# Performance work log

Hardware: AMD Instinct MI355X
Metric: run time of the kernel (lower is better)

Reference implementation:

```python
import jax, jax.numpy as jnp
import numpy as np

B, S, D, H = 2, 2048, 4096, 32
HD = D // H  # 128

def _rope(t, cos, sin):
    # t: [B,S,H,HD]; cos,sin: [S,HD//2]; interleaved complex pairs on last dim
    b, s, h, d = t.shape
    tr = t.reshape(b, s, h, d // 2, 2)
    x0, x1 = tr[..., 0], tr[..., 1]
    c = cos[None, :, None, :]
    sn = sin[None, :, None, :]
    o0 = x0 * c - x1 * sn
    o1 = x0 * sn + x1 * c
    return jnp.stack([o0, o1], axis=-1).reshape(b, s, h, d)

def setup_inputs() -> dict:
    key = jax.random.key(0)
    ks = jax.random.split(key, 6)
    x = jax.random.normal(ks[0], (B, S, D), dtype=jnp.float32)
    theta = 10000.0 ** (-jnp.arange(0, HD, 2, dtype=jnp.float32) / HD)  # [HD//2]
    ang = jnp.arange(S, dtype=jnp.float32)[:, None] * theta[None, :]    # [S, HD//2]
    freqs_cos, freqs_sin = jnp.cos(ang), jnp.sin(ang)
    # additive causal mask [S,S]
    mask = jnp.where(jnp.triu(jnp.ones((S, S), dtype=bool), k=1), -1e9, 0.0).astype(jnp.float32)
    std = 1.0 / np.sqrt(D)
    wq = jax.random.normal(ks[1], (D, D), dtype=jnp.float32) * std
    wk = jax.random.normal(ks[2], (D, D), dtype=jnp.float32) * std
    wv = jax.random.normal(ks[3], (D, D), dtype=jnp.float32) * std
    wo = jax.random.normal(ks[4], (D, D), dtype=jnp.float32) * std
    return {"x": x, "freqs_cos": freqs_cos, "freqs_sin": freqs_sin, "mask": mask,
            "wq": wq, "wk": wk, "wv": wv, "wo": wo, "start_pos": 0}

def reference(x, freqs_cos, freqs_sin, mask, wq, wk, wv, wo, start_pos):
    b, s, d = x.shape
    # Linear layers: torch nn.Linear stores weight [out,in] -> x @ W.T
    xq = (x @ wq.T).reshape(b, s, H, HD)
    xk = (x @ wk.T).reshape(b, s, H, HD)
    xv = (x @ wv.T).reshape(b, s, H, HD)
    xq = _rope(xq, freqs_cos, freqs_sin)
    xk = _rope(xk, freqs_cos, freqs_sin)
    # prefill (start_pos=0): cache slice [:, :s] == xk, xv
    scale = 1.0 / jnp.sqrt(jnp.float32(HD))
    scores = jnp.einsum("bqhd,bkhd->bhqk", xq, xk) * scale + mask[None, None, :, :]
    probs = jax.nn.softmax(scores, axis=-1)
    out = jnp.einsum("bhqk,bkhd->bqhd", probs, xv).reshape(b, s, d)
    return out @ wo.T
```

## Files before the change

### kernel.cpp

```cpp
#include <hip/hip_runtime.h>
#include <hip/hip_bf16.h>
#include <math.h>

typedef unsigned short u16;
typedef __bf16 bf16x8 __attribute__((ext_vector_type(8)));
typedef float f32x4 __attribute__((ext_vector_type(4)));

#define B_  2
#define S_  2048
#define D_  4096
#define H_  32
#define HD_ 128

__device__ __forceinline__ unsigned rne_bf16(float x) {
  unsigned u = __float_as_uint(x);
  return (u + 0x7fffu + ((u >> 16) & 1u)) >> 16;
}

__device__ __forceinline__ void async16(void* lds_p, const void* g) {
  __builtin_amdgcn_global_load_lds(
      (__attribute__((address_space(1))) void*)(g),
      (__attribute__((address_space(3))) void*)(lds_p), 16, 0, 0);
}

__global__ __launch_bounds__(256) void convert_bf16(
    const float* __restrict__ src, u16* __restrict__ dst, int n8) {
  int i = blockIdx.x * 256 + threadIdx.x;
  if (i >= n8) return;
  const float4* s = (const float4*)src + (size_t)i * 2;
  float4 a = s[0], b = s[1];
  uint4 o;
  o.x = rne_bf16(a.x) | (rne_bf16(a.y) << 16);
  o.y = rne_bf16(a.z) | (rne_bf16(a.w) << 16);
  o.z = rne_bf16(b.x) | (rne_bf16(b.y) << 16);
  o.w = rne_bf16(b.z) | (rne_bf16(b.w) << 16);
  ((uint4*)dst)[i] = o;
}

template <int MODE>
__global__ __launch_bounds__(256, 3) void gemm_bt(
    const u16* __restrict__ A, const u16* __restrict__ Bw,
    u16* __restrict__ outB, float* __restrict__ outF,
    const float* __restrict__ fc, const float* __restrict__ fs) {
  __shared__ __align__(16) u16 lds[16384];
  const int tid  = threadIdx.x;
  const int lane = tid & 63;
  const int wave = tid >> 6;
  const int lm   = lane & 15, quad = lane >> 4;
  const int mr = (wave >> 1) * 64, nc = (wave & 1) * 64;
  const int K = 4096;
  const int NT = K / 32;

  const int bid = blockIdx.y * 32 + blockIdx.x;
  const int xg = bid & 7, l = bid >> 3;
  const int m0 = (((xg & 3) * 8) + (l & 7)) * 128;
  const int n0 = (((xg >> 2) * 16) + (l >> 3)) * 128;

  const int ca = tid, cb = tid + 256;
  const int ra = ca >> 2, ga = ((ca & 3) ^ ((ca >> 3) & 3)) * 8;
  const int rb = cb >> 2, gb = ((cb & 3) ^ ((cb >> 3) & 3)) * 8;
  const u16* Ag0 = A + (size_t)(m0 + ra) * K + ga;
  const u16* Ag1 = A + (size_t)(m0 + rb) * K + gb;
  const u16* Bg0 = Bw + (size_t)(n0 + ra) * K + ga;
  const u16* Bg1 = Bw + (size_t)(n0 + rb) * K + gb;

  const int koff = (quad ^ ((lm >> 1) & 3)) * 8;

  f32x4 acc[4][4] = {};

  async16(&lds[ca * 8], Ag0);
  async16(&lds[cb * 8], Ag1);
  async16(&lds[4096 + ca * 8], Bg0);
  async16(&lds[4096 + cb * 8], Bg1);
  __syncthreads();

  for (int t = 0; t < NT; ++t) {
    const u16* As = lds + (t & 1) * 8192;
    const u16* Bs = As + 4096;
    if (t < NT - 1) {
      u16* Ld = lds + ((t + 1) & 1) * 8192;
      const size_t ko = (size_t)(t + 1) * 32;
      async16(&Ld[ca * 8], Ag0 + ko);
      async16(&Ld[cb * 8], Ag1 + ko);
      async16(&Ld[4096 + ca * 8], Bg0 + ko);
      async16(&Ld[4096 + cb * 8], Bg1 + ko);
    }
    bf16x8 af[4], bfr[4];
#pragma unroll
    for (int i = 0; i < 4; ++i) af[i] = *(const bf16x8*)&As[(mr + i * 16 + lm) * 32 + koff];
#pragma unroll
    for (int j = 0; j < 4; ++j) bfr[j] = *(const bf16x8*)&Bs[(nc + j * 16 + lm) * 32 + koff];
#pragma unroll
    for (int i = 0; i < 4; ++i)
#pragma unroll
      for (int j = 0; j < 4; ++j)
        acc[i][j] = __builtin_amdgcn_mfma_f32_16x16x32_bf16(af[i], bfr[j], acc[i][j], 0, 0, 0);
    __syncthreads();
  }

  if (MODE == 1) {
#pragma unroll
    for (int i = 0; i < 4; ++i) {
      const int mbase = m0 + mr + i * 16 + quad * 4;
#pragma unroll
      for (int j = 0; j < 4; ++j) {
        const int n = n0 + nc + j * 16 + lm;
        const int h = n >> 7, d = n & 127, ir = d >> 1;
#pragma unroll
        for (int r = 0; r < 4; ++r) {
          const int m = mbase + r;
          const int s = m & (S_ - 1);
          const int bb = m >> 11;
          float v = acc[i][j][r];
          float p = __shfl_xor(v, 1);
          float cv = fc[s * (HD_ / 2) + ir];
          float sv = fs[s * (HD_ / 2) + ir];
          float o = ((lane & 1) == 0) ? (v * cv - p * sv) : (p * sv + v * cv);
          float po = __shfl_xor(o, 1);
          if ((lane & 1) == 0) {
            unsigned pkt = rne_bf16(o) | (rne_bf16(po) << 16);
            size_t idx = (((size_t)(bb * H_ + h) * S_ + s) * HD_ + d) >> 1;
            ((unsigned*)outB)[idx] = pkt;
          }
        }
      }
    }
  } else if (MODE == 3) {
#pragma unroll
    for (int i = 0; i < 4; ++i) {
      const int mbase = m0 + mr + i * 16 + quad * 4;
      const int s0 = mbase & (S_ - 1);
      const int bb = mbase >> 11;
#pragma unroll
      for (int j = 0; j < 4; ++j) {
        const int n = n0 + nc + j * 16 + lm;
        const int h = n >> 7, d = n & 127;
        uint2 pkt;
        pkt.x = rne_bf16(acc[i][j][0]) | (rne_bf16(acc[i][j][1]) << 16);
        pkt.y = rne_bf16(acc[i][j][2]) | (rne_bf16(acc[i][j][3]) << 16);
        size_t idx = ((size_t)(bb * H_ + h) * HD_ + d) * S_ + s0;
        *(uint2*)&outB[idx] = pkt;
      }
    }
  } else {
#pragma unroll
    for (int i = 0; i < 4; ++i) {
      const int mbase = m0 + mr + i * 16 + quad * 4;
#pragma unroll
      for (int j = 0; j < 4; ++j) {
        const int n = n0 + nc + j * 16 + lm;
#pragma unroll
        for (int r = 0; r < 4; ++r) outF[(size_t)(mbase + r) * D_ + n] = acc[i][j][r];
      }
    }
  }
}

__global__ __launch_bounds__(256, 2) void flash_attn(
    const u16* __restrict__ Qb, const u16* __restrict__ Kb,
    const u16* __restrict__ Vtb, u16* __restrict__ attn) {
  __shared__ __align__(16) u16 lds[32768];

  const int tid = threadIdx.x;
  const int lane = tid & 63, w = tid >> 6;
  const int lm = lane & 15, quad = lane >> 4;
  const int qb = 15 - blockIdx.x;
  const int bh = blockIdx.y;
  const int bb = bh >> 5, h = bh & 31;

  const u16* Qg = Qb + ((size_t)bh * S_ + qb * 128 + w * 32) * HD_;
  const u16* Kg = Kb + (size_t)bh * S_ * HD_;
  const u16* Vg = Vtb + (size_t)bh * HD_ * S_;

  const u16* kp[4];
  const u16* vp[4];
#pragma unroll
  for (int it = 0; it < 4; ++it) {
    int c = tid + 256 * it;
    int kr = c >> 4, kc = (c & 15) ^ (kr & 15);
    kp[it] = Kg + (size_t)kr * HD_ + kc * 8;
    int vr = c >> 3, vc = (c & 7) ^ (vr & 7);
    vp[it] = Vg + (size_t)vr * S_ + vc * 8;
  }

  bf16x8 qf[2][4];
#pragma unroll
  for (int qt = 0; qt < 2; ++qt)
#pragma unroll
    for (int dk = 0; dk < 4; ++dk)
      qf[qt][dk] = *(const bf16x8*)(Qg + (size_t)(qt * 16 + lm) * HD_ + dk * 32 + quad * 8);

  f32x4 accO[8][2] = {};
  float m_run[2] = {-1e30f, -1e30f}, l_run[2] = {0.f, 0.f};
  const float scale = 0.08838834764831845f;
  const int nkt = 2 * qb + 2;
  const int qg0 = qb * 128 + w * 32;
  const int wq_max = qg0 + 31;

#pragma unroll
  for (int it = 0; it < 4; ++it) {
    async16(&lds[(tid + 256 * it) * 8], kp[it]);
    async16(&lds[8192 + (tid + 256 * it) * 8], vp[it]);
  }

  for (int kt = 0; kt < nkt; ++kt) {
    const int k0 = kt * 64;
    const int cur = (kt & 1) * 16384;
    __syncthreads();
    if (kt + 1 < nkt) {
      const int nxt = cur ^ 16384;
      const size_t koK = (size_t)(kt + 1) * 64 * HD_;
      const size_t koV = (size_t)(kt + 1) * 64;
#pragma unroll
      for (int it = 0; it < 4; ++it) {
        async16(&lds[nxt + (tid + 256 * it) * 8], kp[it] + koK);
        async16(&lds[nxt + 8192 + (tid + 256 * it) * 8], vp[it] + koV);
      }
    }
    if (k0 <= wq_max) {
      const u16* Ks = lds + cur;
      const u16* Vts = lds + cur + 8192;
      f32x4 sacc[2][4] = {};
#pragma unroll
      for (int dk = 0; dk < 4; ++dk) {
        bf16x8 kf[4];
#pragma unroll
        for (int t = 0; t < 4; ++t) {
          int row = (t >> 1) * 32 + ((lm >> 2) * 8) + ((t & 1) * 4) + (lm & 3);
          int ch = (dk * 4 + quad) ^ (row & 15);
          kf[t] = *(const bf16x8*)&Ks[(row * 16 + ch) * 8];
        }
#pragma unroll
        for (int t = 0; t < 4; ++t)
#pragma unroll
          for (int qt = 0; qt < 2; ++qt)
            sacc[qt][t] = __builtin_amdgcn_mfma_f32_16x16x32_bf16(kf[t], qf[qt][dk], sacc[qt][t], 0, 0, 0);
      }
      if (k0 + 63 > qg0) {
#pragma unroll
        for (int qt = 0; qt < 2; ++qt) {
          int q = qg0 + qt * 16 + lm;
#pragma unroll
          for (int t = 0; t < 4; ++t) {
            int kb = k0 + (t >> 1) * 32 + quad * 8 + (t & 1) * 4;
#pragma unroll
            for (int r = 0; r < 4; ++r)
              if (kb + r > q) sacc[qt][t][r] = -1e30f;
          }
        }
      }
      bf16x8 pf[2][2];
      float alpha[2];
#pragma unroll
      for (int qt = 0; qt < 2; ++qt) {
        float tmax = sacc[qt][0][0];
#pragma unroll
        for (int t = 0; t < 4; ++t)
#pragma unroll
          for (int r = 0; r < 4; ++r) tmax = fmaxf(tmax, sacc[qt][t][r]);
        tmax = fmaxf(tmax, __shfl_xor(tmax, 16));
        tmax = fmaxf(tmax, __shfl_xor(tmax, 32));
        float mnew = fmaxf(m_run[qt], tmax);
        alpha[qt] = __expf((m_run[qt] - mnew) * scale);
        m_run[qt] = mnew;
        float ms = mnew * scale;
        float rs = 0.f;
#pragma unroll
        for (int t = 0; t < 4; ++t)
#pragma unroll
          for (int r = 0; r < 4; ++r) {
            float p = __expf(fmaf(sacc[qt][t][r], scale, -ms));
            sacc[qt][t][r] = p;
            rs += p;
          }
        rs += __shfl_xor(rs, 16);
        rs += __shfl_xor(rs, 32);
        l_run[qt] = l_run[qt] * alpha[qt] + rs;
#pragma unroll
        for (int kc = 0; kc < 2; ++kc)
#pragma unroll
          for (int j = 0; j < 4; ++j) {
            pf[kc][qt][j]     = (__bf16)sacc[qt][2 * kc][j];
            pf[kc][qt][j + 4] = (__bf16)sacc[qt][2 * kc + 1][j];
          }
      }
#pragma unroll
      for (int dt = 0; dt < 8; ++dt)
#pragma unroll
        for (int qt = 0; qt < 2; ++qt)
#pragma unroll
          for (int r = 0; r < 4; ++r) accO[dt][qt][r] *= alpha[qt];
#pragma unroll
      for (int kc = 0; kc < 2; ++kc)
#pragma unroll
        for (int dt = 0; dt < 8; ++dt) {
          int row = dt * 16 + lm;
          int ch = (kc * 4 + quad) ^ (row & 7);
          bf16x8 vf = *(const bf16x8*)&Vts[(row * 8 + ch) * 8];
#pragma unroll
          for (int qt = 0; qt < 2; ++qt)
            accO[dt][qt] = __builtin_amdgcn_mfma_f32_16x16x32_bf16(vf, pf[kc][qt], accO[dt][qt], 0, 0, 0);
        }
    }
  }

  __syncthreads();
  u16* Et = lds;
  float inv[2] = {1.f / l_run[0], 1.f / l_run[1]};
#pragma unroll
  for (int dt = 0; dt < 8; ++dt)
#pragma unroll
    for (int qt = 0; qt < 2; ++qt) {
      const int rowq = w * 32 + qt * 16 + lm;
#pragma unroll
      for (int rp = 0; rp < 2; ++rp) {
        float a0 = accO[dt][qt][rp * 2] * inv[qt];
        float a1 = accO[dt][qt][rp * 2 + 1] * inv[qt];
        unsigned pkt = rne_bf16(a0) | (rne_bf16(a1) << 16);
        *(unsigned*)&Et[rowq * 136 + dt * 16 + quad * 4 + rp * 2] = pkt;
      }
    }
  const int rloc = w * 32 + (lane >> 1);
  const int half = lane & 1;
  const size_t gbase = (size_t)(bb * S_ + qb * 128 + rloc) * D_ + h * 128 + half * 64;
#pragma unroll
  for (int k = 0; k < 8; ++k) {
    uint4 vv = *(const uint4*)&Et[rloc * 136 + half * 64 + k * 8];
    *(uint4*)&attn[gbase + k * 8] = vv;
  }
}

extern "C" void kernel_launch(void* const* d_in, const int* in_sizes, int n_in,
                              void* d_out, int out_size, void* d_ws, size_t ws_size,
                              hipStream_t stream) {
  const float* x  = (const float*)d_in[0];
  const float* fc = (const float*)d_in[1];
  const float* fs = (const float*)d_in[2];
  const float* wq = (const float*)d_in[4];
  const float* wk = (const float*)d_in[5];
  const float* wv = (const float*)d_in[6];
  const float* wo = (const float*)d_in[7];
  float* out = (float*)d_out;

  char* ws = (char*)d_ws;
  const size_t SZ = (size_t)B_ * S_ * D_ * 2;
  u16* xb  = (u16*)(ws);
  u16* wqb = (u16*)(ws + SZ);
  u16* wkb = (u16*)(ws + 2 * SZ);
  u16* wvb = (u16*)(ws + 3 * SZ);
  u16* Qb  = (u16*)(ws + 4 * SZ);
  u16* Kb  = (u16*)(ws + 5 * SZ);
  u16* Vtb = (u16*)(ws + 6 * SZ);
  u16* attn = xb;
  u16* wob  = wqb;

  dim3 blk(256);
  const int n8 = (B_ * S_ * D_) / 8;
  convert_bf16<<<n8 / 256, blk, 0, stream>>>(x, xb, n8);
  convert_bf16<<<n8 / 256, blk, 0, stream>>>(wq, wqb, n8);
  convert_bf16<<<n8 / 256, blk, 0, stream>>>(wk, wkb, n8);
  convert_bf16<<<n8 / 256, blk, 0, stream>>>(wv, wvb, n8);

  dim3 g1(32, 32);
  gemm_bt<1><<<g1, blk, 0, stream>>>(xb, wqb, Qb, nullptr, fc, fs);
  gemm_bt<1><<<g1, blk, 0, stream>>>(xb, wkb, Kb, nullptr, fc, fs);
  gemm_bt<3><<<g1, blk, 0, stream>>>(xb, wvb, Vtb, nullptr, nullptr, nullptr);

  dim3 g2(16, 64);
  flash_attn<<<g2, blk, 0, stream>>>(Qb, Kb, Vtb, attn);

  convert_bf16<<<n8 / 256, blk, 0, stream>>>(wo, wob, n8);
  gemm_bt<4><<<g1, blk, 0, stream>>>(attn, wob, nullptr, out, nullptr, nullptr);
}
```

Before: 1.126 ms.

## Triple-buffer GEMM loads, lazy softmax rescale, MFMA priority, batch conversions

The GEMM moves from double to triple-buffered LDS staging, prefetching two K-tiles ahead and waiting with explicit vmcnt counts and raw barriers instead of __syncthreads. Flash attention now rescales the running max and accumulators only when any lane's new tile max exceeds the old one by a threshold, and raises wave priority around the MFMA blocks. The four input fp32-to-bf16 conversions are merged into one launch. Together these aim to hide load latency, skip per-tile rescale work and cut launch overhead. The costs are higher LDS use per GEMM block, which may lower occupancy, and the risk that a stale running max lets exp values grow within the threshold bound.

```diff
diff --git a/kernel.cpp b/kernel.cpp
--- a/kernel.cpp
+++ b/kernel.cpp
@@ -37,12 +37,32 @@
   ((uint4*)dst)[i] = o;
 }
 
+__global__ __launch_bounds__(256) void convert_bf16_x4(
+    const float* __restrict__ s0, const float* __restrict__ s1,
+    const float* __restrict__ s2, const float* __restrict__ s3,
+    u16* __restrict__ d0, u16* __restrict__ d1,
+    u16* __restrict__ d2, u16* __restrict__ d3) {
+  const int per = (B_ * S_ * D_) / 8 / 256;
+  const int which = blockIdx.x / per;
+  const int i = (blockIdx.x % per) * 256 + threadIdx.x;
+  const float* src = which == 0 ? s0 : which == 1 ? s1 : which == 2 ? s2 : s3;
+  u16* dst = which == 0 ? d0 : which == 1 ? d1 : which == 2 ? d2 : d3;
+  const float4* s = (const float4*)src + (size_t)i * 2;
+  float4 a = s[0], b = s[1];
+  uint4 o;
+  o.x = rne_bf16(a.x) | (rne_bf16(a.y) << 16);
+  o.y = rne_bf16(a.z) | (rne_bf16(a.w) << 16);
+  o.z = rne_bf16(b.x) | (rne_bf16(b.y) << 16);
+  o.w = rne_bf16(b.z) | (rne_bf16(b.w) << 16);
+  ((uint4*)dst)[i] = o;
+}
+
 template <int MODE>
 __global__ __launch_bounds__(256, 3) void gemm_bt(
     const u16* __restrict__ A, const u16* __restrict__ Bw,
     u16* __restrict__ outB, float* __restrict__ outF,
     const float* __restrict__ fc, const float* __restrict__ fs) {
-  __shared__ __align__(16) u16 lds[16384];
+  __shared__ __align__(16) u16 lds[24576];
   const int tid  = threadIdx.x;
   const int lane = tid & 63;
   const int wave = tid >> 6;
@@ -68,23 +88,25 @@
 
   f32x4 acc[4][4] = {};
 
-  async16(&lds[ca * 8], Ag0);
-  async16(&lds[cb * 8], Ag1);
-  async16(&lds[4096 + ca * 8], Bg0);
-  async16(&lds[4096 + cb * 8], Bg1);
-  __syncthreads();
-
+#define GSTAGE(BUF, T) do {                                   \
+    u16* Ld_ = lds + (BUF) * 8192;                            \
+    const size_t ko_ = (size_t)(T) * 32;                      \
+    async16(&Ld_[ca * 8], Ag0 + ko_);                         \
+    async16(&Ld_[cb * 8], Ag1 + ko_);                         \
+    async16(&Ld_[4096 + ca * 8], Bg0 + ko_);                  \
+    async16(&Ld_[4096 + cb * 8], Bg1 + ko_);                  \
+  } while (0)
+
+  GSTAGE(0, 0);
+  GSTAGE(1, 1);
+  asm volatile("s_waitcnt vmcnt(4)" ::: "memory");
+  asm volatile("s_barrier" ::: "memory");
+
+  int rbuf = 0, sbuf = 2;
   for (int t = 0; t < NT; ++t) {
-    const u16* As = lds + (t & 1) * 8192;
+    const u16* As = lds + rbuf * 8192;
     const u16* Bs = As + 4096;
-    if (t < NT - 1) {
-      u16* Ld = lds + ((t + 1) & 1) * 8192;
-      const size_t ko = (size_t)(t + 1) * 32;
-      async16(&Ld[ca * 8], Ag0 + ko);
-      async16(&Ld[cb * 8], Ag1 + ko);
-      async16(&Ld[4096 + ca * 8], Bg0 + ko);
-      async16(&Ld[4096 + cb * 8], Bg1 + ko);
-    }
+    if (t + 2 < NT) GSTAGE(sbuf, t + 2);
     bf16x8 af[4], bfr[4];
 #pragma unroll
     for (int i = 0; i < 4; ++i) af[i] = *(const bf16x8*)&As[(mr + i * 16 + lm) * 32 + koff];
@@ -95,8 +117,18 @@
 #pragma unroll
       for (int j = 0; j < 4; ++j)
         acc[i][j] = __builtin_amdgcn_mfma_f32_16x16x32_bf16(af[i], bfr[j], acc[i][j], 0, 0, 0);
-    __syncthreads();
-  }
+    if (t < NT - 1) {
+      if (t + 2 < NT) {
+        asm volatile("s_waitcnt vmcnt(4)" ::: "memory");
+      } else {
+        asm volatile("s_waitcnt vmcnt(0)" ::: "memory");
+      }
+      asm volatile("s_barrier" ::: "memory");
+    }
+    rbuf = rbuf == 2 ? 0 : rbuf + 1;
+    sbuf = sbuf == 2 ? 0 : sbuf + 1;
+  }
+#undef GSTAGE
 
   if (MODE == 1) {
 #pragma unroll
@@ -193,6 +225,7 @@
   f32x4 accO[8][2] = {};
   float m_run[2] = {-1e30f, -1e30f}, l_run[2] = {0.f, 0.f};
   const float scale = 0.08838834764831845f;
+  const float THR = 90.50966799187809f;
   const int nkt = 2 * qb + 2;
   const int qg0 = qb * 128 + w * 32;
   const int wq_max = qg0 + 31;
@@ -230,11 +263,13 @@
           int ch = (dk * 4 + quad) ^ (row & 15);
           kf[t] = *(const bf16x8*)&Ks[(row * 16 + ch) * 8];
         }
+        __builtin_amdgcn_s_setprio(1);
 #pragma unroll
         for (int t = 0; t < 4; ++t)
 #pragma unroll
           for (int qt = 0; qt < 2; ++qt)
             sacc[qt][t] = __builtin_amdgcn_mfma_f32_16x16x32_bf16(kf[t], qf[qt][dk], sacc[qt][t], 0, 0, 0);
+        __builtin_amdgcn_s_setprio(0);
       }
       if (k0 + 63 > qg0) {
 #pragma unroll
@@ -249,8 +284,7 @@
           }
         }
       }
-      bf16x8 pf[2][2];
-      float alpha[2];
+      float tmaxv[2];
 #pragma unroll
       for (int qt = 0; qt < 2; ++qt) {
         float tmax = sacc[qt][0][0];
@@ -260,10 +294,26 @@
           for (int r = 0; r < 4; ++r) tmax = fmaxf(tmax, sacc[qt][t][r]);
         tmax = fmaxf(tmax, __shfl_xor(tmax, 16));
         tmax = fmaxf(tmax, __shfl_xor(tmax, 32));
-        float mnew = fmaxf(m_run[qt], tmax);
-        alpha[qt] = __expf((m_run[qt] - mnew) * scale);
-        m_run[qt] = mnew;
-        float ms = mnew * scale;
+        tmaxv[qt] = tmax;
+      }
+      bool needl = (tmaxv[0] - m_run[0] > THR) || (tmaxv[1] - m_run[1] > THR);
+      if (__any(needl)) {
+#pragma unroll
+        for (int qt = 0; qt < 2; ++qt) {
+          float mnew = fmaxf(m_run[qt], tmaxv[qt]);
+          float alpha = __expf((m_run[qt] - mnew) * scale);
+          m_run[qt] = mnew;
+          l_run[qt] *= alpha;
+#pragma unroll
+          for (int dt = 0; dt < 8; ++dt)
+#pragma unroll
+            for (int r = 0; r < 4; ++r) accO[dt][qt][r] *= alpha;
+        }
+      }
+      bf16x8 pf[2][2];
+#pragma unroll
+      for (int qt = 0; qt < 2; ++qt) {
+        float ms = m_run[qt] * scale;
         float rs = 0.f;
 #pragma unroll
         for (int t = 0; t < 4; ++t)
@@ -275,7 +325,7 @@
           }
         rs += __shfl_xor(rs, 16);
         rs += __shfl_xor(rs, 32);
-        l_run[qt] = l_run[qt] * alpha[qt] + rs;
+        l_run[qt] += rs;
 #pragma unroll
         for (int kc = 0; kc < 2; ++kc)
 #pragma unroll
@@ -284,12 +334,7 @@
             pf[kc][qt][j + 4] = (__bf16)sacc[qt][2 * kc + 1][j];
           }
       }
-#pragma unroll
-      for (int dt = 0; dt < 8; ++dt)
-#pragma unroll
-        for (int qt = 0; qt < 2; ++qt)
-#pragma unroll
-          for (int r = 0; r < 4; ++r) accO[dt][qt][r] *= alpha[qt];
+      __builtin_amdgcn_s_setprio(1);
 #pragma unroll
       for (int kc = 0; kc < 2; ++kc)
 #pragma unroll
@@ -301,6 +346,7 @@
           for (int qt = 0; qt < 2; ++qt)
             accO[dt][qt] = __builtin_amdgcn_mfma_f32_16x16x32_bf16(vf, pf[kc][qt], accO[dt][qt], 0, 0, 0);
         }
+      __builtin_amdgcn_s_setprio(0);
     }
   }
 
@@ -356,10 +402,7 @@
 
   dim3 blk(256);
   const int n8 = (B_ * S_ * D_) / 8;
-  convert_bf16<<<n8 / 256, blk, 0, stream>>>(x, xb, n8);
-  convert_bf16<<<n8 / 256, blk, 0, stream>>>(wq, wqb, n8);
-  convert_bf16<<<n8 / 256, blk, 0, stream>>>(wk, wkb, n8);
-  convert_bf16<<<n8 / 256, blk, 0, stream>>>(wv, wvb, n8);
+  convert_bf16_x4<<<4 * (n8 / 256), blk, 0, stream>>>(x, wq, wk, wv, xb, wqb, wkb, wvb);
 
   dim3 g1(32, 32);
   gemm_bt<1><<<g1, blk, 0, stream>>>(xb, wqb, Qb, nullptr, fc, fs);
```

New measurement: 1.135 ms. About the same (+0.9%).
